# Kernel tuning notes

Measured on AMD Instinct MI355X. Metric: run time of the kernel, lower is better.

Reference implementation:

```python
import jax, jax.numpy as jnp
import numpy as np

SEQ, BATCH, HID, OUT, NLAYERS = 2048, 16, 512, 10, 5


def setup_inputs() -> dict:
    key = jax.random.key(0)
    ks = jax.random.split(key, 5)
    scale_in = 1.0 / np.sqrt(HID)
    x = jax.random.normal(ks[0], (SEQ, BATCH, HID), dtype=jnp.float32)
    # Per-layer SRU weights: W maps input -> [x_tilde, f_gate, r_gate] (3H).
    Ws = jax.random.normal(ks[1], (NLAYERS, 3 * HID, HID), dtype=jnp.float32) * scale_in
    # Gate biases: [b_f, b_r] concatenated (2H per layer).
    bs = jax.random.normal(ks[2], (NLAYERS, 2 * HID), dtype=jnp.float32) * 0.1
    fc_W = jax.random.normal(ks[3], (OUT, HID), dtype=jnp.float32) * scale_in
    fc_b = jax.random.normal(ks[4], (OUT,), dtype=jnp.float32) * 0.1
    return {"x": x, "Ws": Ws, "bs": bs, "fc_W": fc_W, "fc_b": fc_b}


def _sru_layer(x, W, b):
    # x: [L, B, H]; W: [3H, H]; b: [2H]
    U = jnp.einsum("lbh,gh->lbg", x, W)  # [L, B, 3H]
    xt, zf, zr = jnp.split(U, 3, axis=-1)
    bf, br = jnp.split(b, 2)
    f = jax.nn.sigmoid(zf + bf)  # forget gate [L, B, H]
    r = jax.nn.sigmoid(zr + br)  # reset/highway gate

    def step(c_prev, inp):
        f_t, xt_t = inp
        c_t = f_t * c_prev + (1.0 - f_t) * xt_t
        return c_t, c_t

    c0 = jnp.zeros(x.shape[1:], dtype=x.dtype)
    _, c = jax.lax.scan(step, c0, (f, xt))  # c: [L, B, H]
    h = r * c + (1.0 - r) * x  # highway connection
    return h


def reference(x, Ws, bs, fc_W, fc_b):
    h = x
    for l in range(NLAYERS):
        h = _sru_layer(h, Ws[l], bs[l])
    out = jnp.einsum("lbh,oh->lbo", h, fc_W) + fc_b
    return out
```

## Files before the change

### kernel.cpp

```cpp
#include <hip/hip_runtime.h>
#include <hip/hip_bf16.h>

#define SEQ 2048
#define BATCH 16
#define HID 512
#define OUT_DIM 10
#define NLAYERS 5
#define M_ROWS (SEQ * BATCH)
#define N3H (3 * HID)
#define GK HID

#define CHUNK 32
#define NSEG (SEQ / CHUNK)

typedef __attribute__((ext_vector_type(8))) _Float16 f16x8;
typedef __attribute__((ext_vector_type(4))) float f32x4;
typedef __attribute__((ext_vector_type(8))) unsigned short u16x8;

__device__ __forceinline__ unsigned short f2h(float x) {
  return __builtin_bit_cast(unsigned short, (_Float16)x);
}
__device__ __forceinline__ float h2f(unsigned short v) {
  return (float)__builtin_bit_cast(_Float16, v);
}

__global__ __launch_bounds__(256) void cvt_f32_to_f16(const float* __restrict__ in,
                                                      unsigned short* __restrict__ out) {
  size_t i = ((size_t)blockIdx.x * 256 + threadIdx.x) * 8;
  float4 a = *(const float4*)(in + i);
  float4 b = *(const float4*)(in + i + 4);
  u16x8 r;
  r[0] = f2h(a.x); r[1] = f2h(a.y); r[2] = f2h(a.z); r[3] = f2h(a.w);
  r[4] = f2h(b.x); r[5] = f2h(b.y); r[6] = f2h(b.z); r[7] = f2h(b.w);
  *(u16x8*)(out + i) = r;
}

__global__ __launch_bounds__(256) void gemm_mfma(const unsigned short* __restrict__ A,
                                                 const unsigned short* __restrict__ B,
                                                 unsigned short* __restrict__ C) {
  __shared__ unsigned short lds[2][8192];
  const int tid = threadIdx.x;
  const int nwg = (M_ROWS / 128) * (N3H / 128);
  const int cpx = nwg / 8;
  const int swz = (blockIdx.x % 8) * cpx + blockIdx.x / 8;
  const int bm = swz / (N3H / 128);
  const int bn = swz % (N3H / 128);
  const int lane = tid & 63;
  const int wid = tid >> 6;
  const int wm = (wid >> 1) * 64, wn = (wid & 1) * 64;

  const unsigned short* Ag = A + (size_t)bm * 128 * GK;
  const unsigned short* Bg = B + (size_t)bn * 128 * GK;

  const int s0 = tid, s1 = tid + 256;
  const int r0 = s0 >> 2, c0 = (s0 & 3) * 8;
  const int r1 = s1 >> 2, c1 = (s1 & 3) * 8;

  const int fr = lane & 15;
  const int ko = (lane >> 4) * 8;

  f32x4 acc[4][4];
#pragma unroll
  for (int i = 0; i < 4; ++i)
#pragma unroll
    for (int j = 0; j < 4; ++j) acc[i][j] = (f32x4){0.f, 0.f, 0.f, 0.f};

#define STAGE(buf, k0)                                                                              \
  {                                                                                                 \
    __builtin_amdgcn_global_load_lds(                                                               \
        (const __attribute__((address_space(1))) void*)(Ag + (size_t)r0 * GK + (k0) + c0),          \
        (__attribute__((address_space(3))) void*)&lds[buf][s0 * 8], 16, 0, 0);                      \
    __builtin_amdgcn_global_load_lds(                                                               \
        (const __attribute__((address_space(1))) void*)(Ag + (size_t)r1 * GK + (k0) + c1),          \
        (__attribute__((address_space(3))) void*)&lds[buf][s1 * 8], 16, 0, 0);                      \
    __builtin_amdgcn_global_load_lds(                                                               \
        (const __attribute__((address_space(1))) void*)(Bg + (size_t)r0 * GK + (k0) + c0),          \
        (__attribute__((address_space(3))) void*)&lds[buf][4096 + s0 * 8], 16, 0, 0);               \
    __builtin_amdgcn_global_load_lds(                                                               \
        (const __attribute__((address_space(1))) void*)(Bg + (size_t)r1 * GK + (k0) + c1),          \
        (__attribute__((address_space(3))) void*)&lds[buf][4096 + s1 * 8], 16, 0, 0);               \
  }

  STAGE(0, 0);
  __syncthreads();
  int cur = 0;
#pragma unroll 1
  for (int kt = 0; kt < GK / 32; ++kt) {
    if (kt + 1 < GK / 32) STAGE(cur ^ 1, (kt + 1) * 32);
    f16x8 af[4], bfr[4];
#pragma unroll
    for (int t = 0; t < 4; ++t) {
      af[t]  = *(const f16x8*)&lds[cur][(wm + t * 16 + fr) * 32 + ko];
      bfr[t] = *(const f16x8*)&lds[cur][4096 + (wn + t * 16 + fr) * 32 + ko];
    }
#pragma unroll
    for (int mt = 0; mt < 4; ++mt)
#pragma unroll
      for (int nt = 0; nt < 4; ++nt)
        acc[mt][nt] = __builtin_amdgcn_mfma_f32_16x16x32_f16(af[mt], bfr[nt], acc[mt][nt], 0, 0, 0);
    if (kt + 1 < GK / 32) {
      __syncthreads();
      cur ^= 1;
    }
  }
#undef STAGE

  __syncthreads();
  unsigned short* cl = &lds[0][0];
  const int er = (lane >> 4) * 4;
#pragma unroll
  for (int mt = 0; mt < 4; ++mt)
#pragma unroll
    for (int nt = 0; nt < 4; ++nt) {
      const int row = wm + mt * 16 + er;
      const int col = wn + nt * 16 + fr;
#pragma unroll
      for (int j = 0; j < 4; ++j) cl[(row + j) * 128 + col] = f2h(acc[mt][nt][j]);
    }
  __syncthreads();
  unsigned short* Cb = C + (size_t)bm * 128 * N3H + bn * 128;
#pragma unroll
  for (int i = 0; i < 8; ++i) {
    int flat = i * 2048 + tid * 8;
    int r = flat >> 7, c = flat & 127;
    *(u16x8*)(Cb + (size_t)r * N3H + c) = *(const u16x8*)&cl[flat];
  }
}

__global__ __launch_bounds__(256) void scan_pass1(const unsigned short* __restrict__ U,
                                                  const float* __restrict__ bias,
                                                  float* __restrict__ Fseg,
                                                  float* __restrict__ Cseg) {
  int t = blockIdx.x * 256 + threadIdx.x;
  int h = t & (HID - 1);
  int b = (t >> 9) & (BATCH - 1);
  int s = t >> 13;
  const float bfv = bias[h];
  const unsigned short* Up = U + (size_t)(s * CHUNK) * BATCH * N3H + (size_t)b * N3H + h;
  float F = 1.f, c = 0.f;
#pragma unroll 8
  for (int i = 0; i < CHUNK; ++i) {
    float xt = h2f(Up[0]);
    float zf = h2f(Up[HID]);
    float f = 1.f / (1.f + __expf(-(zf + bfv)));
    c = f * c + (1.f - f) * xt;
    F *= f;
    Up += BATCH * N3H;
  }
  size_t o = ((size_t)s * BATCH + b) * HID + h;
  Fseg[o] = F;
  Cseg[o] = c;
}

__global__ __launch_bounds__(256) void scan_mid(const float* __restrict__ Fseg,
                                                float* Cseg) {
  int t = blockIdx.x * 256 + threadIdx.x;
  float c = 0.f;
#pragma unroll 4
  for (int s = 0; s < NSEG; ++s) {
    size_t o = (size_t)s * BATCH * HID + t;
    float F = Fseg[o], Cv = Cseg[o];
    Cseg[o] = c;
    c = F * c + Cv;
  }
}

__global__ __launch_bounds__(256) void scan_pass3(const unsigned short* __restrict__ U,
                                                  const float* __restrict__ bias,
                                                  const float* __restrict__ Cin,
                                                  unsigned short* hb) {
  int t = blockIdx.x * 256 + threadIdx.x;
  int h = t & (HID - 1);
  int b = (t >> 9) & (BATCH - 1);
  int s = t >> 13;
  const float bfv = bias[h];
  const float brv = bias[HID + h];
  float c = Cin[(size_t)s * BATCH * HID + (b << 9) + h];
  const unsigned short* Up = U + (size_t)(s * CHUNK) * BATCH * N3H + (size_t)b * N3H + h;
  unsigned short* hp = hb + (size_t)(s * CHUNK) * BATCH * HID + (b << 9) + h;
#pragma unroll 4
  for (int i = 0; i < CHUNK; ++i) {
    float xt = h2f(Up[0]);
    float zf = h2f(Up[HID]);
    float zr = h2f(Up[2 * HID]);
    float xv = h2f(hp[0]);
    float f = 1.f / (1.f + __expf(-(zf + bfv)));
    float r = 1.f / (1.f + __expf(-(zr + brv)));
    c = f * c + (1.f - f) * xt;
    hp[0] = f2h(r * c + (1.f - r) * xv);
    Up += BATCH * N3H;
    hp += BATCH * HID;
  }
}

#define FCR 16
__global__ __launch_bounds__(256) void fc_kernel(const unsigned short* __restrict__ H,
                                                 const float* __restrict__ W,
                                                 const float* __restrict__ bv,
                                                 float* __restrict__ out) {
  __shared__ float hs[FCR][516];
  __shared__ float ws[OUT_DIM][516];
  const int tid = threadIdx.x;
  const size_t m0 = (size_t)blockIdx.x * FCR;
#pragma unroll
  for (int i = 0; i < 4; ++i) {
    int f = tid + i * 256;
    int row = f >> 6;
    int kq = f & 63;
    u16x8 v = *(const u16x8*)(H + (m0 + row) * 512 + kq * 8);
#pragma unroll
    for (int j = 0; j < 8; ++j) hs[row][kq * 8 + j] = h2f(v[j]);
  }
#pragma unroll
  for (int i = 0; i < 5; ++i) {
    int f = tid + i * 256;
    int row = f >> 7;
    int kq = f & 127;
    float4 v = *(const float4*)(W + row * 512 + kq * 4);
    *(float4*)&ws[row][kq * 4] = v;
  }
  __syncthreads();
  if (tid < FCR * OUT_DIM) {
    int row = tid / OUT_DIM;
    int o = tid - row * OUT_DIM;
    float acc = bv[o];
#pragma unroll 8
    for (int k = 0; k < 512; ++k) acc += hs[row][k] * ws[o][k];
    out[(m0 + row) * OUT_DIM + o] = acc;
  }
}

extern "C" void kernel_launch(void* const* d_in, const int* in_sizes, int n_in,
                              void* d_out, int out_size, void* d_ws, size_t ws_size,
                              hipStream_t stream) {
  const float* x   = (const float*)d_in[0];
  const float* Ws  = (const float*)d_in[1];
  const float* bs  = (const float*)d_in[2];
  const float* fcW = (const float*)d_in[3];
  const float* fcb = (const float*)d_in[4];
  float* out = (float*)d_out;

  char* ws = (char*)d_ws;
  const size_t MiB = 1024 * 1024;
  unsigned short* Ub = (unsigned short*)ws;
  unsigned short* hb = (unsigned short*)(ws + 96 * MiB);
  unsigned short* Wh = (unsigned short*)(ws + 128 * MiB);
  float*        Fseg = (float*)(ws + 136 * MiB);
  float*        Cseg = (float*)(ws + 138 * MiB);

  cvt_f32_to_f16<<<(NLAYERS * N3H * HID) / (256 * 8), 256, 0, stream>>>(Ws, Wh);
  cvt_f32_to_f16<<<(M_ROWS * HID) / (256 * 8), 256, 0, stream>>>(x, hb);

  for (int l = 0; l < NLAYERS; ++l) {
    gemm_mfma<<<(M_ROWS / 128) * (N3H / 128), 256, 0, stream>>>(
        hb, Wh + (size_t)l * N3H * HID, Ub);
    const float* bias = bs + (size_t)l * 2 * HID;
    int nthr = BATCH * HID * NSEG;
    scan_pass1<<<nthr / 256, 256, 0, stream>>>(Ub, bias, Fseg, Cseg);
    scan_mid<<<BATCH * HID / 256, 256, 0, stream>>>(Fseg, Cseg);
    scan_pass3<<<nthr / 256, 256, 0, stream>>>(Ub, bias, Cseg, hb);
  }
  fc_kernel<<<M_ROWS / FCR, 256, 0, stream>>>(hb, fcW, fcb, out);
}
```

Measured before the change: 654.8 us.

## Replace double-buffered GEMM with weight-stationary LDS kernel streaming A from global

The per-layer GEMM now loads a 64-column slice of the weight matrix into padded LDS once per block, then processes 512 rows in two passes of 256. The A operand is read straight from global memory into registers with one-step software prefetch. This removes the per-k-step LDS staging of A and the barriers between steps. In exchange, A fragments come from uncoalesced 16-byte per-lane global loads, and C is written as scattered 2-byte stores instead of a coalesced LDS-staged epilogue.

New measurement: 1.305 ms. 99.3% more time.

```diff
diff --git a/kernel.cpp b/kernel.cpp
--- a/kernel.cpp
+++ b/kernel.cpp
@@ -35,95 +35,91 @@
   *(u16x8*)(out + i) = r;
 }
 
-__global__ __launch_bounds__(256) void gemm_mfma(const unsigned short* __restrict__ A,
-                                                 const unsigned short* __restrict__ B,
-                                                 unsigned short* __restrict__ C) {
-  __shared__ unsigned short lds[2][8192];
+__global__ __launch_bounds__(256) void gemm_wstat(const unsigned short* __restrict__ A,
+                                                  const unsigned short* __restrict__ W,
+                                                  unsigned short* __restrict__ C) {
+  __shared__ unsigned short wlds[64][520];
   const int tid = threadIdx.x;
-  const int nwg = (M_ROWS / 128) * (N3H / 128);
+  const int nwg = 64 * 24;
   const int cpx = nwg / 8;
   const int swz = (blockIdx.x % 8) * cpx + blockIdx.x / 8;
-  const int bm = swz / (N3H / 128);
-  const int bn = swz % (N3H / 128);
+  const int bm = swz / 24;
+  const int bn = swz % 24;
   const int lane = tid & 63;
   const int wid = tid >> 6;
-  const int wm = (wid >> 1) * 64, wn = (wid & 1) * 64;
-
-  const unsigned short* Ag = A + (size_t)bm * 128 * GK;
-  const unsigned short* Bg = B + (size_t)bn * 128 * GK;
-
-  const int s0 = tid, s1 = tid + 256;
-  const int r0 = s0 >> 2, c0 = (s0 & 3) * 8;
-  const int r1 = s1 >> 2, c1 = (s1 & 3) * 8;
+
+  {
+    const unsigned short* Wg = W + (size_t)bn * 64 * GK;
+    const int r = tid >> 2;
+    const int q = tid & 3;
+#pragma unroll
+    for (int i = 0; i < 16; ++i) {
+      int k = q * 128 + i * 8;
+      *(u16x8*)&wlds[r][k] = *(const u16x8*)(Wg + (size_t)r * GK + k);
+    }
+  }
+  __syncthreads();
 
   const int fr = lane & 15;
   const int ko = (lane >> 4) * 8;
 
-  f32x4 acc[4][4];
-#pragma unroll
-  for (int i = 0; i < 4; ++i)
-#pragma unroll
-    for (int j = 0; j < 4; ++j) acc[i][j] = (f32x4){0.f, 0.f, 0.f, 0.f};
-
-#define STAGE(buf, k0)                                                                              \
-  {                                                                                                 \
-    __builtin_amdgcn_global_load_lds(                                                               \
-        (const __attribute__((address_space(1))) void*)(Ag + (size_t)r0 * GK + (k0) + c0),          \
-        (__attribute__((address_space(3))) void*)&lds[buf][s0 * 8], 16, 0, 0);                      \
-    __builtin_amdgcn_global_load_lds(                                                               \
-        (const __attribute__((address_space(1))) void*)(Ag + (size_t)r1 * GK + (k0) + c1),          \
-        (__attribute__((address_space(3))) void*)&lds[buf][s1 * 8], 16, 0, 0);                      \
-    __builtin_amdgcn_global_load_lds(                                                               \
-        (const __attribute__((address_space(1))) void*)(Bg + (size_t)r0 * GK + (k0) + c0),          \
-        (__attribute__((address_space(3))) void*)&lds[buf][4096 + s0 * 8], 16, 0, 0);               \
-    __builtin_amdgcn_global_load_lds(                                                               \
-        (const __attribute__((address_space(1))) void*)(Bg + (size_t)r1 * GK + (k0) + c1),          \
-        (__attribute__((address_space(3))) void*)&lds[buf][4096 + s1 * 8], 16, 0, 0);               \
-  }
-
-  STAGE(0, 0);
-  __syncthreads();
-  int cur = 0;
 #pragma unroll 1
-  for (int kt = 0; kt < GK / 32; ++kt) {
-    if (kt + 1 < GK / 32) STAGE(cur ^ 1, (kt + 1) * 32);
-    f16x8 af[4], bfr[4];
-#pragma unroll
-    for (int t = 0; t < 4; ++t) {
-      af[t]  = *(const f16x8*)&lds[cur][(wm + t * 16 + fr) * 32 + ko];
-      bfr[t] = *(const f16x8*)&lds[cur][4096 + (wn + t * 16 + fr) * 32 + ko];
+  for (int p = 0; p < 2; ++p) {
+    const size_t rowg0 = (size_t)bm * 512 + p * 256 + wid * 64;
+    const unsigned short* Ap = A + (rowg0 + fr) * GK + ko;
+
+    f32x4 acc[4][4];
+#pragma unroll
+    for (int i = 0; i < 4; ++i)
+#pragma unroll
+      for (int j = 0; j < 4; ++j) acc[i][j] = (f32x4){0.f, 0.f, 0.f, 0.f};
+
+    f16x8 acur[4];
+#pragma unroll
+    for (int mt = 0; mt < 4; ++mt)
+      acur[mt] = *(const f16x8*)(Ap + (size_t)mt * 16 * GK);
+
+#pragma unroll
+    for (int kt = 0; kt < 15; ++kt) {
+      f16x8 anext[4];
+#pragma unroll
+      for (int mt = 0; mt < 4; ++mt)
+        anext[mt] = *(const f16x8*)(Ap + (size_t)mt * 16 * GK + (kt + 1) * 32);
+      f16x8 wf[4];
+#pragma unroll
+      for (int nt = 0; nt < 4; ++nt)
+        wf[nt] = *(const f16x8*)&wlds[nt * 16 + fr][kt * 32 + ko];
+#pragma unroll
+      for (int mt = 0; mt < 4; ++mt)
+#pragma unroll
+        for (int nt = 0; nt < 4; ++nt)
+          acc[mt][nt] = __builtin_amdgcn_mfma_f32_16x16x32_f16(acur[mt], wf[nt], acc[mt][nt], 0, 0, 0);
+#pragma unroll
+      for (int mt = 0; mt < 4; ++mt) acur[mt] = anext[mt];
     }
+    {
+      f16x8 wf[4];
+#pragma unroll
+      for (int nt = 0; nt < 4; ++nt)
+        wf[nt] = *(const f16x8*)&wlds[nt * 16 + fr][15 * 32 + ko];
+#pragma unroll
+      for (int mt = 0; mt < 4; ++mt)
+#pragma unroll
+        for (int nt = 0; nt < 4; ++nt)
+          acc[mt][nt] = __builtin_amdgcn_mfma_f32_16x16x32_f16(acur[mt], wf[nt], acc[mt][nt], 0, 0, 0);
+    }
+
+    const int er = (lane >> 4) * 4;
 #pragma unroll
     for (int mt = 0; mt < 4; ++mt)
 #pragma unroll
-      for (int nt = 0; nt < 4; ++nt)
-        acc[mt][nt] = __builtin_amdgcn_mfma_f32_16x16x32_f16(af[mt], bfr[nt], acc[mt][nt], 0, 0, 0);
-    if (kt + 1 < GK / 32) {
-      __syncthreads();
-      cur ^= 1;
-    }
-  }
-#undef STAGE
-
-  __syncthreads();
-  unsigned short* cl = &lds[0][0];
-  const int er = (lane >> 4) * 4;
-#pragma unroll
-  for (int mt = 0; mt < 4; ++mt)
-#pragma unroll
-    for (int nt = 0; nt < 4; ++nt) {
-      const int row = wm + mt * 16 + er;
-      const int col = wn + nt * 16 + fr;
-#pragma unroll
-      for (int j = 0; j < 4; ++j) cl[(row + j) * 128 + col] = f2h(acc[mt][nt][j]);
-    }
-  __syncthreads();
-  unsigned short* Cb = C + (size_t)bm * 128 * N3H + bn * 128;
-#pragma unroll
-  for (int i = 0; i < 8; ++i) {
-    int flat = i * 2048 + tid * 8;
-    int r = flat >> 7, c = flat & 127;
-    *(u16x8*)(Cb + (size_t)r * N3H + c) = *(const u16x8*)&cl[flat];
+      for (int nt = 0; nt < 4; ++nt) {
+        const size_t rb = rowg0 + mt * 16 + er;
+        const int cg = bn * 64 + nt * 16 + fr;
+#pragma unroll
+        for (int j = 0; j < 4; ++j)
+          C[(rb + j) * N3H + cg] = f2h(acc[mt][nt][j]);
+      }
   }
 }
 
@@ -252,8 +248,7 @@
   cvt_f32_to_f16<<<(M_ROWS * HID) / (256 * 8), 256, 0, stream>>>(x, hb);
 
   for (int l = 0; l < NLAYERS; ++l) {
-    gemm_mfma<<<(M_ROWS / 128) * (N3H / 128), 256, 0, stream>>>(
-        hb, Wh + (size_t)l * N3H * HID, Ub);
+    gemm_wstat<<<64 * 24, 256, 0, stream>>>(hb, Wh + (size_t)l * N3H * HID, Ub);
     const float* bias = bs + (size_t)l * 2 * HID;
     int nthr = BATCH * HID * NSEG;
     scan_pass1<<<nthr / 256, 256, 0, stream>>>(Ub, bias, Fseg, Cseg);
```

## Fuse three-pass SRU scan into single decoupled-lookback kernel; pad GEMM epilogue LDS

Applied to the files above, without the earlier changes.

Replaces the three scan kernels (per-chunk reduce, sequential mid scan, apply) with one kernel. Each block computes its chunk's aggregate, publishes it through a flagged 64-bit atomic, and walks back over earlier chunks to get its carry-in. Forget gates and x_tilde are kept in registers between the two phases so U is read once for those columns, and accesses use packed 2-element loads. The GEMM epilogue LDS stride is padded to 136 to reduce bank conflicts. The cost is spin-waiting on global atomics, which relies on earlier blocks being scheduled first, plus a memset per layer.

New measurement: 645.9 us. No clear change (-1.4%).

```diff
diff --git a/kernel.cpp b/kernel.cpp
--- a/kernel.cpp
+++ b/kernel.cpp
@@ -23,6 +23,7 @@
 __device__ __forceinline__ float h2f(unsigned short v) {
   return (float)__builtin_bit_cast(_Float16, v);
 }
+__device__ __forceinline__ float sigm(float x) { return 1.f / (1.f + __expf(-x)); }
 
 __global__ __launch_bounds__(256) void cvt_f32_to_f16(const float* __restrict__ in,
                                                       unsigned short* __restrict__ out) {
@@ -38,7 +39,7 @@
 __global__ __launch_bounds__(256) void gemm_mfma(const unsigned short* __restrict__ A,
                                                  const unsigned short* __restrict__ B,
                                                  unsigned short* __restrict__ C) {
-  __shared__ unsigned short lds[2][8192];
+  __shared__ unsigned short lds[2][8704];
   const int tid = threadIdx.x;
   const int nwg = (M_ROWS / 128) * (N3H / 128);
   const int cpx = nwg / 8;
@@ -115,7 +116,7 @@
       const int row = wm + mt * 16 + er;
       const int col = wn + nt * 16 + fr;
 #pragma unroll
-      for (int j = 0; j < 4; ++j) cl[(row + j) * 128 + col] = f2h(acc[mt][nt][j]);
+      for (int j = 0; j < 4; ++j) cl[(row + j) * 136 + col] = f2h(acc[mt][nt][j]);
     }
   __syncthreads();
   unsigned short* Cb = C + (size_t)bm * 128 * N3H + bn * 128;
@@ -123,73 +124,80 @@
   for (int i = 0; i < 8; ++i) {
     int flat = i * 2048 + tid * 8;
     int r = flat >> 7, c = flat & 127;
-    *(u16x8*)(Cb + (size_t)r * N3H + c) = *(const u16x8*)&cl[flat];
-  }
-}
-
-__global__ __launch_bounds__(256) void scan_pass1(const unsigned short* __restrict__ U,
-                                                  const float* __restrict__ bias,
-                                                  float* __restrict__ Fseg,
-                                                  float* __restrict__ Cseg) {
-  int t = blockIdx.x * 256 + threadIdx.x;
-  int h = t & (HID - 1);
-  int b = (t >> 9) & (BATCH - 1);
-  int s = t >> 13;
-  const float bfv = bias[h];
-  const unsigned short* Up = U + (size_t)(s * CHUNK) * BATCH * N3H + (size_t)b * N3H + h;
-  float F = 1.f, c = 0.f;
-#pragma unroll 8
+    *(u16x8*)(Cb + (size_t)r * N3H + c) = *(const u16x8*)&cl[r * 136 + c];
+  }
+}
+
+__global__ __launch_bounds__(256, 4) void sru_scan_fused(
+    const unsigned short* __restrict__ U,
+    const float* __restrict__ bias,
+    unsigned long long* __restrict__ FC,
+    unsigned short* hb) {
+  const int s = blockIdx.x >> 4;
+  const int b = blockIdx.x & 15;
+  const int h0 = threadIdx.x << 1;
+  const float bf0 = bias[h0], bf1 = bias[h0 + 1];
+  const float br0 = bias[HID + h0], br1 = bias[HID + h0 + 1];
+
+  const size_t rowstep = (size_t)BATCH * N3H;
+  const unsigned short* Up = U + ((size_t)(s * CHUNK) * BATCH + b) * N3H + h0;
+
+  unsigned fx0[CHUNK], fx1[CHUNK];
+  float F0 = 1.f, F1 = 1.f, c0 = 0.f, c1 = 0.f;
+#pragma unroll
   for (int i = 0; i < CHUNK; ++i) {
-    float xt = h2f(Up[0]);
-    float zf = h2f(Up[HID]);
-    float f = 1.f / (1.f + __expf(-(zf + bfv)));
-    c = f * c + (1.f - f) * xt;
-    F *= f;
-    Up += BATCH * N3H;
-  }
-  size_t o = ((size_t)s * BATCH + b) * HID + h;
-  Fseg[o] = F;
-  Cseg[o] = c;
-}
-
-__global__ __launch_bounds__(256) void scan_mid(const float* __restrict__ Fseg,
-                                                float* Cseg) {
-  int t = blockIdx.x * 256 + threadIdx.x;
-  float c = 0.f;
-#pragma unroll 4
-  for (int s = 0; s < NSEG; ++s) {
-    size_t o = (size_t)s * BATCH * HID + t;
-    float F = Fseg[o], Cv = Cseg[o];
-    Cseg[o] = c;
-    c = F * c + Cv;
-  }
-}
-
-__global__ __launch_bounds__(256) void scan_pass3(const unsigned short* __restrict__ U,
-                                                  const float* __restrict__ bias,
-                                                  const float* __restrict__ Cin,
-                                                  unsigned short* hb) {
-  int t = blockIdx.x * 256 + threadIdx.x;
-  int h = t & (HID - 1);
-  int b = (t >> 9) & (BATCH - 1);
-  int s = t >> 13;
-  const float bfv = bias[h];
-  const float brv = bias[HID + h];
-  float c = Cin[(size_t)s * BATCH * HID + (b << 9) + h];
-  const unsigned short* Up = U + (size_t)(s * CHUNK) * BATCH * N3H + (size_t)b * N3H + h;
-  unsigned short* hp = hb + (size_t)(s * CHUNK) * BATCH * HID + (b << 9) + h;
-#pragma unroll 4
+    const unsigned short* p = Up + (size_t)i * rowstep;
+    unsigned xt = *(const unsigned*)(p);
+    unsigned zf = *(const unsigned*)(p + HID);
+    unsigned short fh0 = f2h(sigm(h2f((unsigned short)zf) + bf0));
+    unsigned short fh1 = f2h(sigm(h2f((unsigned short)(zf >> 16)) + bf1));
+    float f0 = h2f(fh0), f1 = h2f(fh1);
+    c0 = f0 * c0 + (1.f - f0) * h2f((unsigned short)xt);
+    c1 = f1 * c1 + (1.f - f1) * h2f((unsigned short)(xt >> 16));
+    F0 *= f0; F1 *= f1;
+    fx0[i] = (xt & 0xffffu) | ((unsigned)fh0 << 16);
+    fx1[i] = (xt >> 16) | ((unsigned)fh1 << 16);
+  }
+
+  const size_t ch = ((size_t)s * BATCH + b) * HID + h0;
+  atomicExch(&FC[ch],
+             ((unsigned long long)__builtin_bit_cast(unsigned, c0) << 32) |
+                 __builtin_bit_cast(unsigned, -F0));
+  atomicExch(&FC[ch + 1],
+             ((unsigned long long)__builtin_bit_cast(unsigned, c1) << 32) |
+                 __builtin_bit_cast(unsigned, -F1));
+
+  float ci0 = 0.f, ci1 = 0.f, P0 = 1.f, P1 = 1.f;
+  for (int j = s - 1; j >= 0; --j) {
+    const size_t cj = ((size_t)j * BATCH + b) * HID + h0;
+    unsigned long long v0, v1;
+    do { v0 = atomicAdd(&FC[cj], 0ULL); } while (!(v0 & 0x80000000ULL));
+    do { v1 = atomicAdd(&FC[cj + 1], 0ULL); } while (!(v1 & 0x80000000ULL));
+    float Fj0 = -__builtin_bit_cast(float, (unsigned)v0);
+    float Cj0 = __builtin_bit_cast(float, (unsigned)(v0 >> 32));
+    float Fj1 = -__builtin_bit_cast(float, (unsigned)v1);
+    float Cj1 = __builtin_bit_cast(float, (unsigned)(v1 >> 32));
+    ci0 += P0 * Cj0; P0 *= Fj0;
+    ci1 += P1 * Cj1; P1 *= Fj1;
+    if (P0 == 0.f && P1 == 0.f) break;
+  }
+
+  float cc0 = ci0, cc1 = ci1;
+  const size_t hstep = (size_t)BATCH * HID;
+  unsigned short* hp = hb + ((size_t)(s * CHUNK) * BATCH + b) * HID + h0;
+#pragma unroll
   for (int i = 0; i < CHUNK; ++i) {
-    float xt = h2f(Up[0]);
-    float zf = h2f(Up[HID]);
-    float zr = h2f(Up[2 * HID]);
-    float xv = h2f(hp[0]);
-    float f = 1.f / (1.f + __expf(-(zf + bfv)));
-    float r = 1.f / (1.f + __expf(-(zr + brv)));
-    c = f * c + (1.f - f) * xt;
-    hp[0] = f2h(r * c + (1.f - r) * xv);
-    Up += BATCH * N3H;
-    hp += BATCH * HID;
+    unsigned zr = *(const unsigned*)(Up + (size_t)i * rowstep + 2 * HID);
+    unsigned xv = *(const unsigned*)(hp + (size_t)i * hstep);
+    float f0 = h2f((unsigned short)(fx0[i] >> 16));
+    float f1 = h2f((unsigned short)(fx1[i] >> 16));
+    cc0 = f0 * cc0 + (1.f - f0) * h2f((unsigned short)fx0[i]);
+    cc1 = f1 * cc1 + (1.f - f1) * h2f((unsigned short)fx1[i]);
+    float r0 = sigm(h2f((unsigned short)zr) + br0);
+    float r1 = sigm(h2f((unsigned short)(zr >> 16)) + br1);
+    float hn0 = r0 * cc0 + (1.f - r0) * h2f((unsigned short)xv);
+    float hn1 = r1 * cc1 + (1.f - r1) * h2f((unsigned short)(xv >> 16));
+    *(unsigned*)(hp + (size_t)i * hstep) = (unsigned)f2h(hn0) | ((unsigned)f2h(hn1) << 16);
   }
 }
 
@@ -245,20 +253,16 @@
   unsigned short* Ub = (unsigned short*)ws;
   unsigned short* hb = (unsigned short*)(ws + 96 * MiB);
   unsigned short* Wh = (unsigned short*)(ws + 128 * MiB);
-  float*        Fseg = (float*)(ws + 136 * MiB);
-  float*        Cseg = (float*)(ws + 138 * MiB);
+  unsigned long long* FC = (unsigned long long*)(ws + 136 * MiB);
 
   cvt_f32_to_f16<<<(NLAYERS * N3H * HID) / (256 * 8), 256, 0, stream>>>(Ws, Wh);
   cvt_f32_to_f16<<<(M_ROWS * HID) / (256 * 8), 256, 0, stream>>>(x, hb);
 
   for (int l = 0; l < NLAYERS; ++l) {
+    hipMemsetAsync(FC, 0, (size_t)NSEG * BATCH * HID * 8, stream);
     gemm_mfma<<<(M_ROWS / 128) * (N3H / 128), 256, 0, stream>>>(
         hb, Wh + (size_t)l * N3H * HID, Ub);
-    const float* bias = bs + (size_t)l * 2 * HID;
-    int nthr = BATCH * HID * NSEG;
-    scan_pass1<<<nthr / 256, 256, 0, stream>>>(Ub, bias, Fseg, Cseg);
-    scan_mid<<<BATCH * HID / 256, 256, 0, stream>>>(Fseg, Cseg);
-    scan_pass3<<<nthr / 256, 256, 0, stream>>>(Ub, bias, Cseg, hb);
+    sru_scan_fused<<<NSEG * BATCH, 256, 0, stream>>>(Ub, bs + (size_t)l * 2 * HID, FC, hb);
   }
   fc_kernel<<<M_ROWS / FCR, 256, 0, stream>>>(hb, fcW, fcb, out);
 }
```
